# Kernel optimization log

Hardware: AMD Instinct MI355X
Metric: run time of the kernel (lower is better)

Reference implementation:

```python
import jax, jax.numpy as jnp
import numpy as np

N_QUBITS = 8
N_LAYERS = 4
N_WIRES = N_QUBITS + 1  # circuit uses an extra ancilla wire
B = 16384
D = 512
LN_EPS = 1e-5


def _rx(theta):
    # RX(t) = [[cos(t/2), -i sin(t/2)], [-i sin(t/2), cos(t/2)]]; theta: () or (B,)
    c = jnp.cos(theta / 2).astype(jnp.complex64)
    s = (-1j) * jnp.sin(theta / 2).astype(jnp.complex64)
    return jnp.stack([jnp.stack([c, s], -1), jnp.stack([s, c], -1)], -2)


def _ry(theta):
    c = jnp.cos(theta / 2).astype(jnp.complex64)
    s = jnp.sin(theta / 2).astype(jnp.complex64)
    return jnp.stack([jnp.stack([c, -s], -1), jnp.stack([s, c], -1)], -2)


def _rz(theta):
    # RZ(t) = diag(e^{-it/2}, e^{it/2})
    half = (theta / 2).astype(jnp.complex64)
    em = jnp.exp(-1j * half)
    ep = jnp.exp(1j * half)
    z = jnp.zeros_like(em)
    return jnp.stack([jnp.stack([em, z], -1), jnp.stack([z, ep], -1)], -2)


def _apply_1q(state, U, wire):
    # state: (B,) + (2,)*N_WIRES ; U: (2,2) shared or (B,2,2) per-sample
    ax = 1 + wire
    s = jnp.moveaxis(state, ax, -1)
    if U.ndim == 2:
        s = jnp.einsum('ij,...j->...i', U, s)
    else:
        s = jnp.einsum('bij,b...j->b...i', U, s)
    return jnp.moveaxis(s, -1, ax)


def _cnot(state, c, t):
    # flip target wire t on the control=1 slice of wire c
    s = jnp.moveaxis(state, (1 + c, 1 + t), (-2, -1))
    s = jnp.stack([s[..., 0, :], jnp.flip(s[..., 1, :], axis=-1)], axis=-2)
    return jnp.moveaxis(s, (-2, -1), (1 + c, 1 + t))


def _quantum_circuit(angles, q_weights):
    # angles: (B, N_QUBITS) per-sample data angles; q_weights: (N_LAYERS, N_QUBITS+1)
    b = angles.shape[0]
    state = jnp.zeros((b, 2 ** N_WIRES), jnp.complex64).at[:, 0].set(1.0)
    state = state.reshape((b,) + (2,) * N_WIRES)
    # data encoding: RX, RZ with per-sample angles
    for i in range(N_QUBITS):
        state = _apply_1q(state, _rx(angles[:, i]), i)
        state = _apply_1q(state, _rz(angles[:, i]), i)
    # first variational layer
    for i in range(N_QUBITS):
        state = _apply_1q(state, _rx(q_weights[0, i]), i)
        state = _apply_1q(state, _rz(q_weights[1, i]), i)
    # entangling layers
    for l in range(1, N_LAYERS):
        for i in range(N_QUBITS):
            state = _cnot(state, i, (i + 1) % N_QUBITS)
            state = _apply_1q(state, _ry(q_weights[l, i]), i)
            state = _apply_1q(state, _rz(q_weights[l, i]), i)
        state = _cnot(state, N_QUBITS - 1, N_QUBITS)
        state = _apply_1q(state, _ry(q_weights[l, -1]), N_QUBITS)
    probs = state.real ** 2 + state.imag ** 2
    # <Z_i> = P(q_i=0) - P(q_i=1)
    zs = []
    for i in range(N_QUBITS):
        axes = tuple(1 + j for j in range(N_WIRES) if j != i)
        p = probs.sum(axes)  # (B, 2)
        zs.append(p[:, 0] - p[:, 1])
    return jnp.stack(zs, axis=1)  # (B, N_QUBITS)


def _forward(x, timestep, w_in, b_in, ln_gamma, ln_beta, q_weights, w_out, b_out):
    h = jnp.tanh(x @ w_in.T + b_in)  # (B, 8)
    mu = h.mean(-1, keepdims=True)
    var = ((h - mu) ** 2).mean(-1, keepdims=True)
    h = (h - mu) / jnp.sqrt(var + LN_EPS) * ln_gamma + ln_beta
    angles = h + timestep  # broadcast scalar timestep
    q_out = _quantum_circuit(angles, q_weights)
    out = q_out @ w_out.T + b_out
    return x + out  # input_dim == output_dim -> residual


def setup_inputs() -> dict:
    key = jax.random.key(0)
    ks = jax.random.split(key, 6)
    x = jax.random.normal(ks[0], (B, D), jnp.float32)
    timestep = jax.random.uniform(ks[1], (1,), jnp.float32)
    w_in = jax.random.normal(ks[2], (N_QUBITS, D), jnp.float32) * np.float32(1.0 / np.sqrt(D))
    b_in = jnp.zeros((N_QUBITS,), jnp.float32)
    ln_gamma = jnp.ones((N_QUBITS,), jnp.float32)
    ln_beta = jnp.zeros((N_QUBITS,), jnp.float32)
    q_weights = jax.random.uniform(ks[3], (N_LAYERS, N_QUBITS + 1), jnp.float32, 0.0, 2.0 * np.pi)
    w_out = jax.random.normal(ks[4], (D, N_QUBITS), jnp.float32) * np.float32(1.0 / np.sqrt(N_QUBITS))
    b_out = jnp.zeros((D,), jnp.float32)
    return {'x': x, 'timestep': timestep, 'w_in': w_in, 'b_in': b_in,
            'ln_gamma': ln_gamma, 'ln_beta': ln_beta, 'q_weights': q_weights,
            'w_out': w_out, 'b_out': b_out}


def reference(x, timestep, w_in, b_in, ln_gamma, ln_beta, q_weights, w_out, b_out):
    return _forward(x, timestep, w_in, b_in, ln_gamma, ln_beta, q_weights, w_out, b_out)
```

## Files before the change

kernel.cpp:

```cpp
#include <hip/hip_runtime.h>
#include <math.h>

#define NSAMP 16384
#define ND    512

typedef float f2 __attribute__((ext_vector_type(2)));
__device__ __forceinline__ f2 spl(float x) { return (f2){x, x}; }

template<int CTRL>
__device__ __forceinline__ float dppf(float x) {
  return __int_as_float(__builtin_amdgcn_update_dpp(
      __float_as_int(x), __float_as_int(x), CTRL, 0xF, 0xF, true));
}
template<int CTRL, int RM, int BM>
__device__ __forceinline__ float dppf_keep(float x) {
  return __int_as_float(__builtin_amdgcn_update_dpp(
      __float_as_int(x), __float_as_int(x), CTRL, RM, BM, false));
}
template<int P>
__device__ __forceinline__ float swzf(float x) {
  return __int_as_float(__builtin_amdgcn_ds_swizzle(__float_as_int(x), P));
}
__device__ __forceinline__ float bpermf(int addrB, float x) {
  return __int_as_float(__builtin_amdgcn_ds_bpermute(addrB, __float_as_int(x)));
}

#if __has_builtin(__builtin_amdgcn_permlane16_swap)
#define HAVE_PLSWAP 1
#endif
__device__ __forceinline__ void plswap16(float x, float& a, float& b) {
#ifdef HAVE_PLSWAP
  auto r = __builtin_amdgcn_permlane16_swap(__float_as_uint(x), __float_as_uint(x), false, false);
  a = __uint_as_float(r[0]); b = __uint_as_float(r[1]);
#else
  a = x; b = swzf<0x401F>(x);
#endif
}
__device__ __forceinline__ void plswap32(float x, float& a, float& b) {
#ifdef HAVE_PLSWAP
  auto r = __builtin_amdgcn_permlane32_swap(__float_as_uint(x), __float_as_uint(x), false, false);
  a = __uint_as_float(r[0]); b = __uint_as_float(r[1]);
#else
  a = x; b = __shfl_xor(x, 32, 64);
#endif
}

template<int M>
__device__ __forceinline__ f2 bfly2(f2 x) {
  f2 r;
  if constexpr (M == 1)       { r.x = dppf<0xB1>(x.x);    r.y = dppf<0xB1>(x.y); }
  else if constexpr (M == 2)  { r.x = dppf<0x4E>(x.x);    r.y = dppf<0x4E>(x.y); }
  else if constexpr (M == 8)  { r.x = dppf<0x128>(x.x);   r.y = dppf<0x128>(x.y); }
  else if constexpr (M == 4)  { r.x = swzf<0x101F>(x.x);  r.y = swzf<0x101F>(x.y); }
  else if constexpr (M == 16) { r.x = swzf<0x401F>(x.x);  r.y = swzf<0x401F>(x.y); }
  else                        { r.x = __shfl_xor(x.x, 32, 64); r.y = __shfl_xor(x.y, 32, 64); }
  return r;
}

__device__ __forceinline__ float fold8_allsum(const float* y, int lane) {
  float v4[4];
#pragma unroll
  for (int i = 0; i < 4; ++i) {
    float keep = (lane & 1) ? y[2 * i + 1] : y[2 * i];
    float send = (lane & 1) ? y[2 * i]     : y[2 * i + 1];
    v4[i] = keep + dppf<0xB1>(send);
  }
  float v2[2];
#pragma unroll
  for (int i = 0; i < 2; ++i) {
    float keep = (lane & 2) ? v4[2 * i + 1] : v4[2 * i];
    float send = (lane & 2) ? v4[2 * i]     : v4[2 * i + 1];
    v2[i] = keep + dppf<0x4E>(send);
  }
  float keep = (lane & 4) ? v2[1] : v2[0];
  float send = (lane & 4) ? v2[0] : v2[1];
  float r = keep + swzf<0x101F>(send);
  r += dppf<0x128>(r);
  { float a, b; plswap16(r, a, b); r = a + b; }
  { float a, b; plswap32(r, a, b); r = a + b; }
  return r;
}

__device__ __forceinline__ float grp8_sum(float x) {
  x += dppf<0xB1>(x);
  x += dppf<0x4E>(x);
  x += swzf<0x101F>(x);
  return x;
}

__device__ __forceinline__ f2 cmul(f2 a, f2 b) {
  f2 bs = __builtin_shufflevector(b, b, 1, 0);
  f2 t  = (f2){-a.y, a.y} * bs;
  return spl(a.x) * b + t;
}

template<int LB>
__device__ __forceinline__ void ry_local(f2* s, float c, float sv) {
#pragma unroll
  for (int r0 = 0; r0 < 8; ++r0) {
    if (r0 & (1 << LB)) continue;
    const int r1 = r0 | (1 << LB);
    f2 a0 = s[r0], a1 = s[r1];
    s[r0] = spl(c) * a0 - spl(sv) * a1;
    s[r1] = spl(sv) * a0 + spl(c) * a1;
  }
}
template<int LB>
__device__ __forceinline__ void rz_local(f2* s, f2 phm, f2 php) {
#pragma unroll
  for (int r = 0; r < 8; ++r) s[r] = cmul(s[r], (r & (1 << LB)) ? php : phm);
}
template<int M>
__device__ __forceinline__ void ry_lane(f2* s, float c, float se) {
#pragma unroll
  for (int r = 0; r < 8; ++r) {
    f2 p = bfly2<M>(s[r]);
    s[r] = spl(c) * s[r] + spl(se) * p;
  }
}
template<int CB, int TB>
__device__ __forceinline__ void cnot_ll(f2* s) {
#pragma unroll
  for (int r0 = 0; r0 < 8; ++r0) {
    if (!(r0 & (1 << CB)) || (r0 & (1 << TB))) continue;
    const int r1 = r0 | (1 << TB);
    f2 t = s[r0]; s[r0] = s[r1]; s[r1] = t;
  }
}
template<int CB, int TM>
__device__ __forceinline__ void cnot_lt(f2* s) {
#pragma unroll
  for (int r = 0; r < 8; ++r) {
    if (!(r & (1 << CB))) continue;
    s[r] = bfly2<TM>(s[r]);
  }
}
__device__ __forceinline__ void cnot_bperm(f2* s, int addrB) {
#pragma unroll
  for (int r = 0; r < 8; ++r) {
    s[r].x = bpermf(addrB, s[r].x);
    s[r].y = bpermf(addrB, s[r].y);
  }
}
__device__ __forceinline__ void cnot_m4_t1(f2* s) {
#pragma unroll
  for (int r = 0; r < 8; ++r) {
    s[r].x = dppf_keep<0xB1, 0xF, 0xA>(s[r].x);
    s[r].y = dppf_keep<0xB1, 0xF, 0xA>(s[r].y);
  }
}
__device__ __forceinline__ void cnot_m1_t2(f2* s) {
#pragma unroll
  for (int r = 0; r < 8; ++r) {
    s[r].x = dppf<0x6C>(s[r].x);
    s[r].y = dppf<0x6C>(s[r].y);
  }
}
template<int TB>
__device__ __forceinline__ void cnot_tl(f2* s, bool cc) {
#pragma unroll
  for (int r0 = 0; r0 < 8; ++r0) {
    if (r0 & (1 << TB)) continue;
    const int r1 = r0 | (1 << TB);
    f2 n0, n1;
    n0.x = cc ? s[r1].x : s[r0].x;  n0.y = cc ? s[r1].y : s[r0].y;
    n1.x = cc ? s[r0].x : s[r1].x;  n1.y = cc ? s[r0].y : s[r1].y;
    s[r0] = n0; s[r1] = n1;
  }
}

__global__ void qpre_kernel(const float* __restrict__ qw, float* __restrict__ ws) {
  int t = threadIdx.x;
  if (t < 27) {
    float s, c; __sincosf(qw[9 + t] * 0.5f, &s, &c);
    ws[2 * t] = c; ws[2 * t + 1] = s;
  }
}

template<bool PRE>
struct Consts {
  const float* qw; const float* ws;
  __device__ __forceinline__ f2 ltrig(int l, int i) const {
    if constexpr (PRE) {
      return ((const f2*)ws)[(l - 1) * 9 + i];
    } else {
      float s, c; __sincosf(qw[l * 9 + i] * 0.5f, &s, &c);
      return (f2){c, s};
    }
  }
};

template<bool PRE, int MODE>
__device__ __forceinline__ void do_layer(f2* st, int lane, const Consts<PRE>& cst, int l,
                                         int addr56, int addr67, int addr78) {
  f2 t[9];
#pragma unroll
  for (int i = 0; i < 9; ++i) t[i] = cst.ltrig(l, i);

  cnot_ll<0, 1>(st);
  ry_local<0>(st, t[0].x, t[0].y);
  rz_local<0>(st, (f2){t[0].x, -t[0].y}, (f2){t[0].x, t[0].y});
  cnot_ll<1, 2>(st);
  ry_local<1>(st, t[1].x, t[1].y);
  cnot_lt<2, 4>(st);
  ry_local<2>(st, t[2].x, t[2].y);
  cnot_m4_t1(st);
  { float se = (lane & 4) ? t[3].y : -t[3].y;
    ry_lane<4>(st, t[3].x, se); }
  cnot_m1_t2(st);
  { float se = (lane & 1) ? t[4].y : -t[4].y;
    ry_lane<1>(st, t[4].x, se); }
  cnot_bperm(st, addr56);
  { float se = (lane & 2) ? t[5].y : -t[5].y;
    ry_lane<2>(st, t[5].x, se); }
  cnot_bperm(st, addr67);
  { float se = (lane & 8) ? t[6].y : -t[6].y;
    ry_lane<8>(st, t[6].x, se); }
  cnot_tl<0>(st, (lane & 16) != 0);
  { float se = (lane & 16) ? t[7].y : -t[7].y;
    ry_lane<16>(st, t[7].x, se); }

  if constexpr (MODE == 1) {
    const float wsel = (lane & 32) ? ((lane & 16) ? t[8].x : t[8].y)
                                   : ((lane & 16) ? -t[8].y : t[8].x);
#pragma unroll
    for (int r = 0; r < 8; ++r) st[r] = st[r] * spl(wsel);
  }
  if constexpr (MODE == 2) {
    cnot_bperm(st, addr78);
  }
  if constexpr (MODE != 3) {
    f2 L4[4];
#pragma unroll
    for (int k = 0; k < 4; ++k) {
      f2 p1 = (f2){t[1].x, (k & 1) ? t[1].y : -t[1].y};
      f2 p2 = (f2){t[2].x, (k & 2) ? t[2].y : -t[2].y};
      L4[k] = cmul(p1, p2);
    }
    f2 phW = (f2){t[3].x, (lane & 4)  ? t[3].y : -t[3].y};
    phW = cmul(phW, (f2){t[4].x, (lane & 1)  ? t[4].y : -t[4].y});
    phW = cmul(phW, (f2){t[5].x, (lane & 2)  ? t[5].y : -t[5].y});
    phW = cmul(phW, (f2){t[6].x, (lane & 8)  ? t[6].y : -t[6].y});
    phW = cmul(phW, (f2){t[7].x, (lane & 16) ? t[7].y : -t[7].y});
    f2 pr[4];
#pragma unroll
    for (int k = 0; k < 4; ++k) pr[k] = cmul(L4[k], phW);
#pragma unroll
    for (int r = 0; r < 8; ++r) st[r] = cmul(st[r], pr[(r >> 1) & 3]);
  }
}

template<bool PRE>
__global__ __launch_bounds__(256, 4) void qlayer_kernel(
    const float* __restrict__ x, const float* __restrict__ tstep,
    const float* __restrict__ w_in, const float* __restrict__ b_in,
    const float* __restrict__ g, const float* __restrict__ be,
    const float* __restrict__ qw, const float* __restrict__ w_out,
    const float* __restrict__ b_out, float* __restrict__ out,
    const float* __restrict__ ws)
{
  __shared__ __align__(16) float s_u[4][8][4];
  __shared__ __align__(16) float s_z[4][8];

  const int tid    = threadIdx.x;
  const int lane   = tid & 63;
  const int wv     = tid >> 6;
  const int sample = blockIdx.x * 4 + wv;
  const int jq     = lane & 7;
  const int dbase  = lane << 3;

  const int addr56 = (lane ^ ((lane & 2) << 2)) << 2;
  const int addr67 = (lane ^ ((lane & 8) << 1)) << 2;
  const int addr78 = (lane ^ ((lane & 16) << 1)) << 2;

  const float4* xr4 = (const float4*)(x + (size_t)sample * ND + dbase);
  const float4 xa = xr4[0], xb = xr4[1];
  const f2 xp0 = (f2){xa.x, xa.y}, xp1 = (f2){xa.z, xa.w};
  const f2 xp2 = (f2){xb.x, xb.y}, xp3 = (f2){xb.z, xb.w};

  float h[8];
#pragma unroll
  for (int j = 0; j < 8; ++j) {
    const float4* wj = (const float4*)(w_in + j * ND + dbase);
    float4 wa = wj[0], wb = wj[1];
    f2 acc = xp0 * (f2){wa.x, wa.y};
    acc += xp1 * (f2){wa.z, wa.w};
    acc += xp2 * (f2){wb.x, wb.y};
    acc += xp3 * (f2){wb.z, wb.w};
    h[j] = acc.x + acc.y;
  }
  const float H = fold8_allsum(h, lane);

  const float t0 = tstep[0];
  float tj;
  {
    float v = H + b_in[jq];
    v = fminf(15.f, fmaxf(-15.f, v));
    float e2 = __expf(2.f * v);
    tj = (e2 - 1.f) * __builtin_amdgcn_rcpf(e2 + 1.f);
  }
  const float mu = grp8_sum(tj) * 0.125f;
  const float dv = tj - mu;
  const float var = grp8_sum(dv * dv) * 0.125f;
  const float rstd = rsqrtf(var + 1e-5f);
  const float ang = dv * rstd * g[jq] + be[jq] + t0;

  {
    float sa, ca; __sincosf(ang * 0.5f, &sa, &ca);
    f2 v0 = spl(ca) * (f2){ca, -sa};
    f2 v1 = spl(sa) * (f2){sa, -ca};
    float s0, c0, s1, c1;
    __sincosf(qw[jq] * 0.5f, &s0, &c0);
    __sincosf(qw[9 + jq] * 0.5f, &s1, &c1);
    f2 M00 = (f2){ c1 * c0, -s1 * c0};
    f2 M01 = (f2){-s1 * s0, -c1 * s0};
    f2 M10 = (f2){ s1 * s0, -c1 * s0};
    f2 M11 = (f2){ c1 * c0,  s1 * c0};
    f2 u0 = cmul(M00, v0) + cmul(M01, v1);
    f2 u1 = cmul(M10, v0) + cmul(M11, v1);
    if (lane < 8) {
      float4 uu = {u0.x, u0.y, u1.x, u1.y};
      *(float4*)&s_u[wv][jq][0] = uu;
    }
  }
  asm volatile("s_waitcnt lgkmcnt(0)" ::: "memory");
  __builtin_amdgcn_sched_barrier(0);

  f2 u0a[3], u1a[3];
#pragma unroll
  for (int i = 0; i < 3; ++i) {
    float4 uu = *(const float4*)&s_u[wv][i][0];
    u0a[i] = (f2){uu.x, uu.y};
    u1a[i] = (f2){uu.z, uu.w};
  }
  f2 hl;
  {
    const f2* ub = (const f2*)&s_u[wv][0][0];
    f2 r4 = ub[4 * 2 + ((lane >> 0) & 1)];
    f2 r5 = ub[5 * 2 + ((lane >> 1) & 1)];
    f2 r3 = ub[3 * 2 + ((lane >> 2) & 1)];
    f2 r6 = ub[6 * 2 + ((lane >> 3) & 1)];
    f2 r7 = ub[7 * 2 + ((lane >> 4) & 1)];
    hl = cmul(cmul(cmul(cmul(r4, r5), r3), r6), r7);
  }
  f2 t01[4];
#pragma unroll
  for (int q = 0; q < 4; ++q)
    t01[q] = cmul((q & 1) ? u1a[0] : u0a[0], (q & 2) ? u1a[1] : u0a[1]);
  f2 st[8];
#pragma unroll
  for (int r = 0; r < 8; ++r)
    st[r] = cmul(cmul(t01[r & 3], (r & 4) ? u1a[2] : u0a[2]), hl);

  Consts<PRE> cst{qw, ws};
  do_layer<PRE, 1>(st, lane, cst, 1, addr56, addr67, addr78);
  do_layer<PRE, 2>(st, lane, cst, 2, addr56, addr67, addr78);
  do_layer<PRE, 3>(st, lane, cst, 3, addr56, addr67, addr78);

  float p[8];
#pragma unroll
  for (int r = 0; r < 8; ++r) p[r] = st[r].x * st[r].x + st[r].y * st[r].y;
  float tot = 0.f;
#pragma unroll
  for (int r = 0; r < 8; ++r) tot += p[r];

  float y[8];
  y[0] = (p[0] - p[1]) + (p[2] - p[3]) + (p[4] - p[5]) + (p[6] - p[7]);
  y[1] = (p[0] + p[1]) - (p[2] + p[3]) + (p[4] + p[5]) - (p[6] + p[7]);
  y[2] = (p[0] + p[1] + p[2] + p[3]) - (p[4] + p[5] + p[6] + p[7]);
  y[3] = (lane & 4)  ? -tot : tot;
  y[4] = (lane & 1)  ? -tot : tot;
  y[5] = (lane & 2)  ? -tot : tot;
  y[6] = (lane & 8)  ? -tot : tot;
  y[7] = (lane & 16) ? -tot : tot;
  const float Z = fold8_allsum(y, lane);
  if (lane < 8) s_z[wv][jq] = Z;
  asm volatile("s_waitcnt lgkmcnt(0)" ::: "memory");
  __builtin_amdgcn_sched_barrier(0);

  float4 za = *(const float4*)&s_z[wv][0];
  float4 zb = *(const float4*)&s_z[wv][4];

  const f2 z01 = (f2){za.x, za.y}, z23 = (f2){za.z, za.w};
  const f2 z45 = (f2){zb.x, zb.y}, z67 = (f2){zb.z, zb.w};
  const float4* wo = (const float4*)(w_out + (size_t)dbase * 8);
  const float4* bo = (const float4*)(b_out + dbase);
  const float4 b0 = bo[0], b1 = bo[1];
  const float xk[8] = {xa.x, xa.y, xa.z, xa.w, xb.x, xb.y, xb.z, xb.w};
  const float bk[8] = {b0.x, b0.y, b0.z, b0.w, b1.x, b1.y, b1.z, b1.w};
  float o[8];
#pragma unroll
  for (int k = 0; k < 8; ++k) {
    float4 wa = wo[2 * k];
    float4 wb = wo[2 * k + 1];
    f2 acc = z01 * (f2){wa.x, wa.y};
    acc += z23 * (f2){wa.z, wa.w};
    acc += z45 * (f2){wb.x, wb.y};
    acc += z67 * (f2){wb.z, wb.w};
    o[k] = xk[k] + bk[k] + acc.x + acc.y;
  }
  float4* outp = (float4*)(out + (size_t)sample * ND + dbase);
  outp[0] = (float4){o[0], o[1], o[2], o[3]};
  outp[1] = (float4){o[4], o[5], o[6], o[7]};
}

extern "C" void kernel_launch(void* const* d_in, const int* in_sizes, int n_in,
                              void* d_out, int out_size, void* d_ws, size_t ws_size,
                              hipStream_t stream) {
  const float* x     = (const float*)d_in[0];
  const float* ts    = (const float*)d_in[1];
  const float* w_in  = (const float*)d_in[2];
  const float* b_in  = (const float*)d_in[3];
  const float* g     = (const float*)d_in[4];
  const float* be    = (const float*)d_in[5];
  const float* qw    = (const float*)d_in[6];
  const float* w_out = (const float*)d_in[7];
  const float* b_out = (const float*)d_in[8];
  float* out = (float*)d_out;

  const bool pre = (d_ws != nullptr) && (ws_size >= 256);
  if (pre) {
    qpre_kernel<<<dim3(1), dim3(64), 0, stream>>>(qw, (float*)d_ws);
    qlayer_kernel<true><<<dim3(NSAMP / 4), dim3(256), 0, stream>>>(
        x, ts, w_in, b_in, g, be, qw, w_out, b_out, out, (const float*)d_ws);
  } else {
    qlayer_kernel<false><<<dim3(NSAMP / 4), dim3(256), 0, stream>>>(
        x, ts, w_in, b_in, g, be, qw, w_out, b_out, out, (const float*)d_ws);
  }
}
```

Measured before the change: 58.18 us.

## Process two samples per wavefront to amortize weight loads and shuffles

Each wavefront now simulates two samples instead of one, holding 16 complex amplitudes per lane. The w_in and w_out loads and the gate constants are shared across both samples, and the two reductions are interleaved for ILP. The grid is halved. This doubles register pressure under launch_bounds(256,4), which could cause spills or lower occupancy.

```diff
diff --git a/kernel.cpp b/kernel.cpp
--- a/kernel.cpp
+++ b/kernel.cpp
@@ -57,28 +57,40 @@
   return r;
 }
 
-__device__ __forceinline__ float fold8_allsum(const float* y, int lane) {
-  float v4[4];
+__device__ __forceinline__ void fold8_allsum2(const float* yA, const float* yB,
+                                              int lane, float& rA, float& rB) {
+  float a4[4], b4[4];
 #pragma unroll
   for (int i = 0; i < 4; ++i) {
-    float keep = (lane & 1) ? y[2 * i + 1] : y[2 * i];
-    float send = (lane & 1) ? y[2 * i]     : y[2 * i + 1];
-    v4[i] = keep + dppf<0xB1>(send);
-  }
-  float v2[2];
+    float kA = (lane & 1) ? yA[2 * i + 1] : yA[2 * i];
+    float sA = (lane & 1) ? yA[2 * i]     : yA[2 * i + 1];
+    float kB = (lane & 1) ? yB[2 * i + 1] : yB[2 * i];
+    float sB = (lane & 1) ? yB[2 * i]     : yB[2 * i + 1];
+    a4[i] = kA + dppf<0xB1>(sA);
+    b4[i] = kB + dppf<0xB1>(sB);
+  }
+  float a2[2], b2[2];
 #pragma unroll
   for (int i = 0; i < 2; ++i) {
-    float keep = (lane & 2) ? v4[2 * i + 1] : v4[2 * i];
-    float send = (lane & 2) ? v4[2 * i]     : v4[2 * i + 1];
-    v2[i] = keep + dppf<0x4E>(send);
-  }
-  float keep = (lane & 4) ? v2[1] : v2[0];
-  float send = (lane & 4) ? v2[0] : v2[1];
-  float r = keep + swzf<0x101F>(send);
-  r += dppf<0x128>(r);
-  { float a, b; plswap16(r, a, b); r = a + b; }
-  { float a, b; plswap32(r, a, b); r = a + b; }
-  return r;
+    float kA = (lane & 2) ? a4[2 * i + 1] : a4[2 * i];
+    float sA = (lane & 2) ? a4[2 * i]     : a4[2 * i + 1];
+    float kB = (lane & 2) ? b4[2 * i + 1] : b4[2 * i];
+    float sB = (lane & 2) ? b4[2 * i]     : b4[2 * i + 1];
+    a2[i] = kA + dppf<0x4E>(sA);
+    b2[i] = kB + dppf<0x4E>(sB);
+  }
+  float kA = (lane & 4) ? a2[1] : a2[0];
+  float sA = (lane & 4) ? a2[0] : a2[1];
+  float kB = (lane & 4) ? b2[1] : b2[0];
+  float sB = (lane & 4) ? b2[0] : b2[1];
+  rA = kA + swzf<0x101F>(sA);
+  rB = kB + swzf<0x101F>(sB);
+  rA += dppf<0x128>(rA);
+  rB += dppf<0x128>(rB);
+  { float a, b; plswap16(rA, a, b); rA = a + b; }
+  { float a, b; plswap16(rB, a, b); rB = a + b; }
+  { float a, b; plswap32(rA, a, b); rA = a + b; }
+  { float a, b; plswap32(rB, a, b); rB = a + b; }
 }
 
 __device__ __forceinline__ float grp8_sum(float x) {
@@ -97,8 +109,8 @@
 template<int LB>
 __device__ __forceinline__ void ry_local(f2* s, float c, float sv) {
 #pragma unroll
-  for (int r0 = 0; r0 < 8; ++r0) {
-    if (r0 & (1 << LB)) continue;
+  for (int r0 = 0; r0 < 16; ++r0) {
+    if ((r0 & 7) & (1 << LB)) continue;
     const int r1 = r0 | (1 << LB);
     f2 a0 = s[r0], a1 = s[r1];
     s[r0] = spl(c) * a0 - spl(sv) * a1;
@@ -108,12 +120,12 @@
 template<int LB>
 __device__ __forceinline__ void rz_local(f2* s, f2 phm, f2 php) {
 #pragma unroll
-  for (int r = 0; r < 8; ++r) s[r] = cmul(s[r], (r & (1 << LB)) ? php : phm);
+  for (int r = 0; r < 16; ++r) s[r] = cmul(s[r], ((r & 7) & (1 << LB)) ? php : phm);
 }
 template<int M>
 __device__ __forceinline__ void ry_lane(f2* s, float c, float se) {
 #pragma unroll
-  for (int r = 0; r < 8; ++r) {
+  for (int r = 0; r < 16; ++r) {
     f2 p = bfly2<M>(s[r]);
     s[r] = spl(c) * s[r] + spl(se) * p;
   }
@@ -121,8 +133,8 @@
 template<int CB, int TB>
 __device__ __forceinline__ void cnot_ll(f2* s) {
 #pragma unroll
-  for (int r0 = 0; r0 < 8; ++r0) {
-    if (!(r0 & (1 << CB)) || (r0 & (1 << TB))) continue;
+  for (int r0 = 0; r0 < 16; ++r0) {
+    if (!((r0 & 7) & (1 << CB)) || ((r0 & 7) & (1 << TB))) continue;
     const int r1 = r0 | (1 << TB);
     f2 t = s[r0]; s[r0] = s[r1]; s[r1] = t;
   }
@@ -130,28 +142,28 @@
 template<int CB, int TM>
 __device__ __forceinline__ void cnot_lt(f2* s) {
 #pragma unroll
-  for (int r = 0; r < 8; ++r) {
-    if (!(r & (1 << CB))) continue;
+  for (int r = 0; r < 16; ++r) {
+    if (!((r & 7) & (1 << CB))) continue;
     s[r] = bfly2<TM>(s[r]);
   }
 }
 __device__ __forceinline__ void cnot_bperm(f2* s, int addrB) {
 #pragma unroll
-  for (int r = 0; r < 8; ++r) {
+  for (int r = 0; r < 16; ++r) {
     s[r].x = bpermf(addrB, s[r].x);
     s[r].y = bpermf(addrB, s[r].y);
   }
 }
 __device__ __forceinline__ void cnot_m4_t1(f2* s) {
 #pragma unroll
-  for (int r = 0; r < 8; ++r) {
+  for (int r = 0; r < 16; ++r) {
     s[r].x = dppf_keep<0xB1, 0xF, 0xA>(s[r].x);
     s[r].y = dppf_keep<0xB1, 0xF, 0xA>(s[r].y);
   }
 }
 __device__ __forceinline__ void cnot_m1_t2(f2* s) {
 #pragma unroll
-  for (int r = 0; r < 8; ++r) {
+  for (int r = 0; r < 16; ++r) {
     s[r].x = dppf<0x6C>(s[r].x);
     s[r].y = dppf<0x6C>(s[r].y);
   }
@@ -159,8 +171,8 @@
 template<int TB>
 __device__ __forceinline__ void cnot_tl(f2* s, bool cc) {
 #pragma unroll
-  for (int r0 = 0; r0 < 8; ++r0) {
-    if (r0 & (1 << TB)) continue;
+  for (int r0 = 0; r0 < 16; ++r0) {
+    if ((r0 & 7) & (1 << TB)) continue;
     const int r1 = r0 | (1 << TB);
     f2 n0, n1;
     n0.x = cc ? s[r1].x : s[r0].x;  n0.y = cc ? s[r1].y : s[r0].y;
@@ -224,7 +236,7 @@
     const float wsel = (lane & 32) ? ((lane & 16) ? t[8].x : t[8].y)
                                    : ((lane & 16) ? -t[8].y : t[8].x);
 #pragma unroll
-    for (int r = 0; r < 8; ++r) st[r] = st[r] * spl(wsel);
+    for (int r = 0; r < 16; ++r) st[r] = st[r] * spl(wsel);
   }
   if constexpr (MODE == 2) {
     cnot_bperm(st, addr78);
@@ -246,7 +258,7 @@
 #pragma unroll
     for (int k = 0; k < 4; ++k) pr[k] = cmul(L4[k], phW);
 #pragma unroll
-    for (int r = 0; r < 8; ++r) st[r] = cmul(st[r], pr[(r >> 1) & 3]);
+    for (int r = 0; r < 16; ++r) st[r] = cmul(st[r], pr[((r & 7) >> 1) & 3]);
   }
 }
 
@@ -259,13 +271,14 @@
     const float* __restrict__ b_out, float* __restrict__ out,
     const float* __restrict__ ws)
 {
-  __shared__ __align__(16) float s_u[4][8][4];
-  __shared__ __align__(16) float s_z[4][8];
+  __shared__ __align__(16) float s_u[4][2][8][4];
+  __shared__ __align__(16) float s_z[4][2][8];
 
   const int tid    = threadIdx.x;
   const int lane   = tid & 63;
   const int wv     = tid >> 6;
-  const int sample = blockIdx.x * 4 + wv;
+  const int smpA   = blockIdx.x * 8 + wv * 2;
+  const int smpB   = smpA + 1;
   const int jq     = lane & 7;
   const int dbase  = lane << 3;
 
@@ -273,42 +286,51 @@
   const int addr67 = (lane ^ ((lane & 8) << 1)) << 2;
   const int addr78 = (lane ^ ((lane & 16) << 1)) << 2;
 
-  const float4* xr4 = (const float4*)(x + (size_t)sample * ND + dbase);
-  const float4 xa = xr4[0], xb = xr4[1];
-  const f2 xp0 = (f2){xa.x, xa.y}, xp1 = (f2){xa.z, xa.w};
-  const f2 xp2 = (f2){xb.x, xb.y}, xp3 = (f2){xb.z, xb.w};
-
-  float h[8];
+  const float4* xrA = (const float4*)(x + (size_t)smpA * ND + dbase);
+  const float4* xrB = (const float4*)(x + (size_t)smpB * ND + dbase);
+  const float4 xaA = xrA[0], xbA = xrA[1];
+  const float4 xaB = xrB[0], xbB = xrB[1];
+  const f2 a0 = (f2){xaA.x, xaA.y}, a1 = (f2){xaA.z, xaA.w};
+  const f2 a2 = (f2){xbA.x, xbA.y}, a3 = (f2){xbA.z, xbA.w};
+  const f2 b0 = (f2){xaB.x, xaB.y}, b1 = (f2){xaB.z, xaB.w};
+  const f2 b2 = (f2){xbB.x, xbB.y}, b3 = (f2){xbB.z, xbB.w};
+
+  float hA[8], hB[8];
 #pragma unroll
   for (int j = 0; j < 8; ++j) {
     const float4* wj = (const float4*)(w_in + j * ND + dbase);
     float4 wa = wj[0], wb = wj[1];
-    f2 acc = xp0 * (f2){wa.x, wa.y};
-    acc += xp1 * (f2){wa.z, wa.w};
-    acc += xp2 * (f2){wb.x, wb.y};
-    acc += xp3 * (f2){wb.z, wb.w};
-    h[j] = acc.x + acc.y;
-  }
-  const float H = fold8_allsum(h, lane);
-
-  const float t0 = tstep[0];
-  float tj;
+    f2 w0 = (f2){wa.x, wa.y}, w1 = (f2){wa.z, wa.w};
+    f2 w2 = (f2){wb.x, wb.y}, w3 = (f2){wb.z, wb.w};
+    f2 accA = a0 * w0 + a1 * w1 + a2 * w2 + a3 * w3;
+    f2 accB = b0 * w0 + b1 * w1 + b2 * w2 + b3 * w3;
+    hA[j] = accA.x + accA.y;
+    hB[j] = accB.x + accB.y;
+  }
+  float HA, HB;
+  fold8_allsum2(hA, hB, lane, HA, HB);
+
+  const float t0  = tstep[0];
+  const float bj  = b_in[jq];
+  const float gj  = g[jq];
+  const float bej = be[jq];
+  float tjA, tjB;
   {
-    float v = H + b_in[jq];
-    v = fminf(15.f, fmaxf(-15.f, v));
-    float e2 = __expf(2.f * v);
-    tj = (e2 - 1.f) * __builtin_amdgcn_rcpf(e2 + 1.f);
-  }
-  const float mu = grp8_sum(tj) * 0.125f;
-  const float dv = tj - mu;
-  const float var = grp8_sum(dv * dv) * 0.125f;
-  const float rstd = rsqrtf(var + 1e-5f);
-  const float ang = dv * rstd * g[jq] + be[jq] + t0;
+    float vA = fminf(15.f, fmaxf(-15.f, HA + bj));
+    float vB = fminf(15.f, fmaxf(-15.f, HB + bj));
+    float eA = __expf(2.f * vA), eB = __expf(2.f * vB);
+    tjA = (eA - 1.f) * __builtin_amdgcn_rcpf(eA + 1.f);
+    tjB = (eB - 1.f) * __builtin_amdgcn_rcpf(eB + 1.f);
+  }
+  const float muA = grp8_sum(tjA) * 0.125f;
+  const float muB = grp8_sum(tjB) * 0.125f;
+  const float dvA = tjA - muA, dvB = tjB - muB;
+  const float varA = grp8_sum(dvA * dvA) * 0.125f;
+  const float varB = grp8_sum(dvB * dvB) * 0.125f;
+  const float angA = dvA * rsqrtf(varA + 1e-5f) * gj + bej + t0;
+  const float angB = dvB * rsqrtf(varB + 1e-5f) * gj + bej + t0;
 
   {
-    float sa, ca; __sincosf(ang * 0.5f, &sa, &ca);
-    f2 v0 = spl(ca) * (f2){ca, -sa};
-    f2 v1 = spl(sa) * (f2){sa, -ca};
     float s0, c0, s1, c1;
     __sincosf(qw[jq] * 0.5f, &s0, &c0);
     __sincosf(qw[9 + jq] * 0.5f, &s1, &c1);
@@ -316,92 +338,116 @@
     f2 M01 = (f2){-s1 * s0, -c1 * s0};
     f2 M10 = (f2){ s1 * s0, -c1 * s0};
     f2 M11 = (f2){ c1 * c0,  s1 * c0};
-    f2 u0 = cmul(M00, v0) + cmul(M01, v1);
-    f2 u1 = cmul(M10, v0) + cmul(M11, v1);
-    if (lane < 8) {
-      float4 uu = {u0.x, u0.y, u1.x, u1.y};
-      *(float4*)&s_u[wv][jq][0] = uu;
+    float saA, caA; __sincosf(angA * 0.5f, &saA, &caA);
+    float saB, caB; __sincosf(angB * 0.5f, &saB, &caB);
+    f2 v0A = spl(caA) * (f2){caA, -saA};
+    f2 v1A = spl(saA) * (f2){saA, -caA};
+    f2 v0B = spl(caB) * (f2){caB, -saB};
+    f2 v1B = spl(saB) * (f2){saB, -caB};
+    f2 u0A = cmul(M00, v0A) + cmul(M01, v1A);
+    f2 u1A = cmul(M10, v0A) + cmul(M11, v1A);
+    f2 u0B = cmul(M00, v0B) + cmul(M01, v1B);
+    f2 u1B = cmul(M10, v0B) + cmul(M11, v1B);
+    if (lane < 16) {
+      const int sb = lane >> 3;
+      f2 u0 = sb ? u0B : u0A;
+      f2 u1 = sb ? u1B : u1A;
+      *(float4*)&s_u[wv][sb][jq][0] = (float4){u0.x, u0.y, u1.x, u1.y};
     }
   }
   asm volatile("s_waitcnt lgkmcnt(0)" ::: "memory");
   __builtin_amdgcn_sched_barrier(0);
 
-  f2 u0a[3], u1a[3];
-#pragma unroll
-  for (int i = 0; i < 3; ++i) {
-    float4 uu = *(const float4*)&s_u[wv][i][0];
-    u0a[i] = (f2){uu.x, uu.y};
-    u1a[i] = (f2){uu.z, uu.w};
-  }
-  f2 hl;
-  {
-    const f2* ub = (const f2*)&s_u[wv][0][0];
+  f2 st[16];
+#pragma unroll
+  for (int smp = 0; smp < 2; ++smp) {
+    const f2* ub = (const f2*)&s_u[wv][smp][0][0];
     f2 r4 = ub[4 * 2 + ((lane >> 0) & 1)];
     f2 r5 = ub[5 * 2 + ((lane >> 1) & 1)];
     f2 r3 = ub[3 * 2 + ((lane >> 2) & 1)];
     f2 r6 = ub[6 * 2 + ((lane >> 3) & 1)];
     f2 r7 = ub[7 * 2 + ((lane >> 4) & 1)];
-    hl = cmul(cmul(cmul(cmul(r4, r5), r3), r6), r7);
-  }
-  f2 t01[4];
-#pragma unroll
-  for (int q = 0; q < 4; ++q)
-    t01[q] = cmul((q & 1) ? u1a[0] : u0a[0], (q & 2) ? u1a[1] : u0a[1]);
-  f2 st[8];
-#pragma unroll
-  for (int r = 0; r < 8; ++r)
-    st[r] = cmul(cmul(t01[r & 3], (r & 4) ? u1a[2] : u0a[2]), hl);
+    f2 hl = cmul(cmul(cmul(cmul(r4, r5), r3), r6), r7);
+    f2 u0q0 = ub[0], u1q0 = ub[1], u0q1 = ub[2], u1q1 = ub[3];
+    f2 u0q2 = ub[4], u1q2 = ub[5];
+    f2 t01[4];
+#pragma unroll
+    for (int q = 0; q < 4; ++q)
+      t01[q] = cmul((q & 1) ? u1q0 : u0q0, (q & 2) ? u1q1 : u0q1);
+#pragma unroll
+    for (int r = 0; r < 8; ++r)
+      st[smp * 8 + r] = cmul(cmul(t01[r & 3], (r & 4) ? u1q2 : u0q2), hl);
+  }
 
   Consts<PRE> cst{qw, ws};
   do_layer<PRE, 1>(st, lane, cst, 1, addr56, addr67, addr78);
   do_layer<PRE, 2>(st, lane, cst, 2, addr56, addr67, addr78);
   do_layer<PRE, 3>(st, lane, cst, 3, addr56, addr67, addr78);
 
-  float p[8];
-#pragma unroll
-  for (int r = 0; r < 8; ++r) p[r] = st[r].x * st[r].x + st[r].y * st[r].y;
-  float tot = 0.f;
-#pragma unroll
-  for (int r = 0; r < 8; ++r) tot += p[r];
-
-  float y[8];
-  y[0] = (p[0] - p[1]) + (p[2] - p[3]) + (p[4] - p[5]) + (p[6] - p[7]);
-  y[1] = (p[0] + p[1]) - (p[2] + p[3]) + (p[4] + p[5]) - (p[6] + p[7]);
-  y[2] = (p[0] + p[1] + p[2] + p[3]) - (p[4] + p[5] + p[6] + p[7]);
-  y[3] = (lane & 4)  ? -tot : tot;
-  y[4] = (lane & 1)  ? -tot : tot;
-  y[5] = (lane & 2)  ? -tot : tot;
-  y[6] = (lane & 8)  ? -tot : tot;
-  y[7] = (lane & 16) ? -tot : tot;
-  const float Z = fold8_allsum(y, lane);
-  if (lane < 8) s_z[wv][jq] = Z;
+  float pA[8], pB[8];
+#pragma unroll
+  for (int r = 0; r < 8; ++r) {
+    pA[r] = st[r].x * st[r].x + st[r].y * st[r].y;
+    pB[r] = st[8 + r].x * st[8 + r].x + st[8 + r].y * st[8 + r].y;
+  }
+  float totA = 0.f, totB = 0.f;
+#pragma unroll
+  for (int r = 0; r < 8; ++r) { totA += pA[r]; totB += pB[r]; }
+
+  float yA[8], yB[8];
+  yA[0] = (pA[0] - pA[1]) + (pA[2] - pA[3]) + (pA[4] - pA[5]) + (pA[6] - pA[7]);
+  yB[0] = (pB[0] - pB[1]) + (pB[2] - pB[3]) + (pB[4] - pB[5]) + (pB[6] - pB[7]);
+  yA[1] = (pA[0] + pA[1]) - (pA[2] + pA[3]) + (pA[4] + pA[5]) - (pA[6] + pA[7]);
+  yB[1] = (pB[0] + pB[1]) - (pB[2] + pB[3]) + (pB[4] + pB[5]) - (pB[6] + pB[7]);
+  yA[2] = (pA[0] + pA[1] + pA[2] + pA[3]) - (pA[4] + pA[5] + pA[6] + pA[7]);
+  yB[2] = (pB[0] + pB[1] + pB[2] + pB[3]) - (pB[4] + pB[5] + pB[6] + pB[7]);
+  yA[3] = (lane & 4)  ? -totA : totA;  yB[3] = (lane & 4)  ? -totB : totB;
+  yA[4] = (lane & 1)  ? -totA : totA;  yB[4] = (lane & 1)  ? -totB : totB;
+  yA[5] = (lane & 2)  ? -totA : totA;  yB[5] = (lane & 2)  ? -totB : totB;
+  yA[6] = (lane & 8)  ? -totA : totA;  yB[6] = (lane & 8)  ? -totB : totB;
+  yA[7] = (lane & 16) ? -totA : totA;  yB[7] = (lane & 16) ? -totB : totB;
+  float ZA, ZB;
+  fold8_allsum2(yA, yB, lane, ZA, ZB);
+  if (lane < 16) {
+    const int sb = lane >> 3;
+    s_z[wv][sb][jq] = sb ? ZB : ZA;
+  }
   asm volatile("s_waitcnt lgkmcnt(0)" ::: "memory");
   __builtin_amdgcn_sched_barrier(0);
 
-  float4 za = *(const float4*)&s_z[wv][0];
-  float4 zb = *(const float4*)&s_z[wv][4];
-
-  const f2 z01 = (f2){za.x, za.y}, z23 = (f2){za.z, za.w};
-  const f2 z45 = (f2){zb.x, zb.y}, z67 = (f2){zb.z, zb.w};
+  const float4 zaA = *(const float4*)&s_z[wv][0][0];
+  const float4 zbA = *(const float4*)&s_z[wv][0][4];
+  const float4 zaB = *(const float4*)&s_z[wv][1][0];
+  const float4 zbB = *(const float4*)&s_z[wv][1][4];
+
+  const f2 zA01 = (f2){zaA.x, zaA.y}, zA23 = (f2){zaA.z, zaA.w};
+  const f2 zA45 = (f2){zbA.x, zbA.y}, zA67 = (f2){zbA.z, zbA.w};
+  const f2 zB01 = (f2){zaB.x, zaB.y}, zB23 = (f2){zaB.z, zaB.w};
+  const f2 zB45 = (f2){zbB.x, zbB.y}, zB67 = (f2){zbB.z, zbB.w};
   const float4* wo = (const float4*)(w_out + (size_t)dbase * 8);
   const float4* bo = (const float4*)(b_out + dbase);
-  const float4 b0 = bo[0], b1 = bo[1];
-  const float xk[8] = {xa.x, xa.y, xa.z, xa.w, xb.x, xb.y, xb.z, xb.w};
-  const float bk[8] = {b0.x, b0.y, b0.z, b0.w, b1.x, b1.y, b1.z, b1.w};
-  float o[8];
+  const float4 bo0 = bo[0], bo1 = bo[1];
+  const float xkA[8] = {xaA.x, xaA.y, xaA.z, xaA.w, xbA.x, xbA.y, xbA.z, xbA.w};
+  const float xkB[8] = {xaB.x, xaB.y, xaB.z, xaB.w, xbB.x, xbB.y, xbB.z, xbB.w};
+  const float bk[8]  = {bo0.x, bo0.y, bo0.z, bo0.w, bo1.x, bo1.y, bo1.z, bo1.w};
+  float oA[8], oB[8];
 #pragma unroll
   for (int k = 0; k < 8; ++k) {
     float4 wa = wo[2 * k];
     float4 wb = wo[2 * k + 1];
-    f2 acc = z01 * (f2){wa.x, wa.y};
-    acc += z23 * (f2){wa.z, wa.w};
-    acc += z45 * (f2){wb.x, wb.y};
-    acc += z67 * (f2){wb.z, wb.w};
-    o[k] = xk[k] + bk[k] + acc.x + acc.y;
-  }
-  float4* outp = (float4*)(out + (size_t)sample * ND + dbase);
-  outp[0] = (float4){o[0], o[1], o[2], o[3]};
-  outp[1] = (float4){o[4], o[5], o[6], o[7]};
+    f2 w01 = (f2){wa.x, wa.y}, w23 = (f2){wa.z, wa.w};
+    f2 w45 = (f2){wb.x, wb.y}, w67 = (f2){wb.z, wb.w};
+    f2 accA = zA01 * w01 + zA23 * w23 + zA45 * w45 + zA67 * w67;
+    f2 accB = zB01 * w01 + zB23 * w23 + zB45 * w45 + zB67 * w67;
+    oA[k] = xkA[k] + bk[k] + accA.x + accA.y;
+    oB[k] = xkB[k] + bk[k] + accB.x + accB.y;
+  }
+  float4* outA = (float4*)(out + (size_t)smpA * ND + dbase);
+  float4* outB = (float4*)(out + (size_t)smpB * ND + dbase);
+  outA[0] = (float4){oA[0], oA[1], oA[2], oA[3]};
+  outA[1] = (float4){oA[4], oA[5], oA[6], oA[7]};
+  outB[0] = (float4){oB[0], oB[1], oB[2], oB[3]};
+  outB[1] = (float4){oB[4], oB[5], oB[6], oB[7]};
 }
 
 extern "C" void kernel_launch(void* const* d_in, const int* in_sizes, int n_in,
@@ -421,10 +467,10 @@
   const bool pre = (d_ws != nullptr) && (ws_size >= 256);
   if (pre) {
     qpre_kernel<<<dim3(1), dim3(64), 0, stream>>>(qw, (float*)d_ws);
-    qlayer_kernel<true><<<dim3(NSAMP / 4), dim3(256), 0, stream>>>(
+    qlayer_kernel<true><<<dim3(NSAMP / 8), dim3(256), 0, stream>>>(
         x, ts, w_in, b_in, g, be, qw, w_out, b_out, out, (const float*)d_ws);
   } else {
-    qlayer_kernel<false><<<dim3(NSAMP / 4), dim3(256), 0, stream>>>(
+    qlayer_kernel<false><<<dim3(NSAMP / 8), dim3(256), 0, stream>>>(
         x, ts, w_in, b_in, g, be, qw, w_out, b_out, out, (const float*)d_ws);
   }
 }
```

Measured after the change: 56.54 us (median of 2 runs). -2.8%, faster.
